# Optimization experiments

Hardware: AMD Instinct MI355X
Metric: run time of the kernel (lower is better)

The kernel has to match this reference:

```python
import jax, jax.numpy as jnp
import numpy as np
from jax import lax

EPS = 1e-5
N_CROPS = 501
CROP_W = 500
RF = 65          # temporal receptive field
KS = 15          # conv1 kernel size
POOL = 3


def _bn(x, g, b, m, v, axis=1):
    shp = [1] * x.ndim
    shp[axis] = -1
    inv = g.reshape(shp) / jnp.sqrt(v.reshape(shp) + EPS)
    return (x - m.reshape(shp)) * inv + b.reshape(shp)


def setup_inputs() -> dict:
    key = jax.random.key(0)
    ks = jax.random.split(key, 16)
    B, C_IN, CH, T = 16, 1, 22, 1001
    F = 36
    OUT = 4
    FLAT = F * 43  # 1548 (corrected fc in_features; repo constant 504 is inconsistent)
    d = {
        "x": jax.random.normal(ks[0], (B, C_IN, CH, T), jnp.float32),
        # temporal conv [1,65]
        "w_t": jax.random.normal(ks[1], (F, 1, 1, RF), jnp.float32) * 0.1,
        "b_t": jax.random.normal(ks[2], (F,), jnp.float32) * 0.1,
        "bn_t_g": jax.random.uniform(ks[3], (F,), jnp.float32, 0.5, 1.5),
        "bn_t_b": jax.random.normal(ks[4], (F,), jnp.float32) * 0.1,
        "bn_t_m": jax.random.normal(ks[5], (F,), jnp.float32) * 0.1,
        "bn_t_v": jax.random.uniform(ks[6], (F,), jnp.float32, 0.5, 1.5),
        # spatial conv [22,1]
        "w_s": jax.random.normal(ks[7], (F, F, CH, 1), jnp.float32) * 0.05,
        "b_s": jax.random.normal(ks[8], (F,), jnp.float32) * 0.1,
        "bn_s_g": jax.random.uniform(ks[9], (F,), jnp.float32, 0.5, 1.5),
        "bn_s_b": jax.random.normal(ks[10], (F,), jnp.float32) * 0.1,
        "bn_s_m": jax.random.normal(ks[11], (F,), jnp.float32) * 0.1,
        "bn_s_v": jax.random.uniform(ks[12], (F,), jnp.float32, 0.5, 1.5),
        # conv1 [1,15] (as 1-D conv over time)
        "w_c": jax.random.normal(ks[13], (F, F, KS), jnp.float32) * 0.05,
        "b_c": jax.random.normal(ks[14], (F,), jnp.float32) * 0.1,
        "bn_c_g": jnp.ones((F,), jnp.float32),
        "bn_c_b": jnp.zeros((F,), jnp.float32),
        "bn_c_m": jnp.zeros((F,), jnp.float32),
        "bn_c_v": jnp.ones((F,), jnp.float32),
        # fc
        "w_fc": jax.random.normal(ks[15], (OUT, FLAT), jnp.float32) * 0.02,
        "b_fc": jnp.zeros((OUT,), jnp.float32),
    }
    return d


def reference(x, w_t, b_t, bn_t_g, bn_t_b, bn_t_m, bn_t_v,
              w_s, b_s, bn_s_g, bn_s_b, bn_s_m, bn_s_v,
              w_c, b_c, bn_c_g, bn_c_b, bn_c_m, bn_c_v,
              w_fc, b_fc):
    B = x.shape[0]
    F = w_t.shape[0]
    OUT = b_fc.shape[0]

    # temporal + spatial conv/BN/ELU are shift-invariant -> compute once over full T
    h = lax.conv_general_dilated(x, w_t, (1, 1), 'VALID',
                                 dimension_numbers=('NCHW', 'OIHW', 'NCHW'))
    h = h + b_t[None, :, None, None]                       # [B,36,22,937]
    h = jax.nn.elu(_bn(h, bn_t_g, bn_t_b, bn_t_m, bn_t_v))
    h = lax.conv_general_dilated(h, w_s, (1, 1), 'VALID',
                                 dimension_numbers=('NCHW', 'OIHW', 'NCHW'))
    h = h + b_s[None, :, None, None]                       # [B,36,1,937]
    h = jax.nn.elu(_bn(h, bn_s_g, bn_s_b, bn_s_m, bn_s_v))
    h = h[:, :, 0, :]                                      # [B,36,937]

    TW = CROP_W - RF + 1  # 436: temporal width of each crop after temporal conv

    def crop_logits(i):
        sl = lax.dynamic_slice_in_dim(h, i, TW, axis=2)    # [B,36,436]
        p1 = sl[:, :, :435].reshape(B, F, 145, POOL).mean(-1)  # avgpool1 -> [B,36,145]
        c = lax.conv_general_dilated(p1, w_c, (1,), 'VALID',
                                     dimension_numbers=('NCH', 'OIH', 'NCH'))
        c = c + b_c[None, :, None]                          # [B,36,131]
        c = jax.nn.elu(_bn(c, bn_c_g, bn_c_b, bn_c_m, bn_c_v))
        p2 = c[:, :, :129].reshape(B, F, 43, POOL).mean(-1)  # avgpool2 -> [B,36,43]
        flat = p2.reshape(B, -1)                            # [B,1548]
        return flat @ w_fc.T + b_fc                         # [B,OUT]

    def step(acc, i):
        return acc + crop_logits(i), None

    init = jnp.zeros((B, OUT), x.dtype)
    total, _ = lax.scan(step, init, jnp.arange(N_CROPS))
    return total / N_CROPS
```

## Files before the change

### kernel.cpp

```cpp
#include <hip/hip_runtime.h>

#define EPS 1e-5f
#define B 16
#define CH 22
#define T_IN 1001
#define F 36
#define RF 65
#define T1 937
#define FC 792
#define KW 99
#define UN 885
#define PSTR 1072
#define PSPAN 304
#define KS 15
#define GN 295
#define WN 129
#define M43 43
#define BF 576

#define H2_OFF  0
#define P_OFF   539712
#define EP_OFF  1157184
#define S_OFF   5235264
#define WTT_OFF 5260032
#define WST_OFF 5262372
#define WCT_OFF 5290884
#define BN_OFF  5310324
#define H1_OFF  5310592

__device__ __forceinline__ float elu_f(float v) {
    return v > 0.f ? v : (__expf(v) - 1.f);
}

__global__ __launch_bounds__(256) void k_prep(
    const float* __restrict__ w_t, const float* __restrict__ w_s,
    const float* __restrict__ w_c,
    const float* __restrict__ b_t, const float* __restrict__ g_t,
    const float* __restrict__ be_t,const float* __restrict__ m_t,
    const float* __restrict__ v_t,
    const float* __restrict__ b_s, const float* __restrict__ g_s,
    const float* __restrict__ be_s,const float* __restrict__ m_s,
    const float* __restrict__ v_s,
    const float* __restrict__ b_c, const float* __restrict__ g_c,
    const float* __restrict__ be_c,const float* __restrict__ m_c,
    const float* __restrict__ v_c,
    float* __restrict__ wtT, float* __restrict__ wsT,
    float* __restrict__ wcT, float* __restrict__ bnz)
{
    int i = blockIdx.x * 256 + threadIdx.x;
    if (i < F * RF)     { int k = i / F,  fi = i % F; wtT[i] = w_t[fi * RF + k]; }
    if (i < FC * F)     { int fc = i / F, fo = i % F; wsT[i] = w_s[fo * FC + fc]; }
    if (i < F * KS * F) { int fk = i / F, fo = i % F; int f = fk / KS, k = fk % KS;
                          wcT[i] = w_c[(fo * F + f) * KS + k]; }
    if (i < F) {
        float s1 = g_t[i] * rsqrtf(v_t[i] + EPS);
        bnz[i]          = s1;
        bnz[F + i]      = (b_t[i] - m_t[i]) * s1 + be_t[i];
        float s2 = g_s[i] * rsqrtf(v_s[i] + EPS);
        bnz[2 * F + i]  = s2;
        bnz[3 * F + i]  = (b_s[i] - m_s[i]) * s2 + be_s[i];
        float s3 = g_c[i] * rsqrtf(v_c[i] + EPS);
        bnz[4 * F + i]  = s3;
        bnz[5 * F + i]  = (b_c[i] - m_c[i]) * s3 + be_c[i];
    }
}

__global__ __launch_bounds__(256) void k_tconv(
    const float* __restrict__ x, const float* __restrict__ wtT,
    const float* __restrict__ bnz, float* __restrict__ h1,
    int t_base, int TS, int TSeff)
{
    const int tloc = blockIdx.x * 256 + threadIdx.x;
    const int b = blockIdx.z, ch = blockIdx.y;
    int t = t_base + tloc;
    int tc = t < (T1 - 1) ? t : (T1 - 1);
    const float* xp = x + (b * CH + ch) * T_IN + tc;

    float acc[F];
    #pragma unroll
    for (int j = 0; j < F; ++j) acc[j] = 0.f;

    #pragma unroll 5
    for (int k = 0; k < RF; ++k) {
        float xv = xp[k];
        const float* wr = wtT + k * F;
        #pragma unroll
        for (int j = 0; j < F; ++j) acc[j] += xv * wr[j];
    }

    if (tloc < TSeff) {
        #pragma unroll
        for (int j = 0; j < F; ++j) {
            float s1 = bnz[j], o1 = bnz[F + j];
            h1[((size_t)(b * F + j) * CH + ch) * TS + tloc] =
                elu_f(acc[j] * s1 + o1);
        }
    }
}

__global__ __launch_bounds__(512) void k_sconv(
    const float* __restrict__ h1, const float* __restrict__ wsT,
    const float* __restrict__ bnz, float* __restrict__ h2,
    int t_base, int TS, int TSeff)
{
    __shared__ float Ls[8 * F * 64];
    const int tid = threadIdx.x;
    const int lane = tid & 63;
    const int w = __builtin_amdgcn_readfirstlane(tid >> 6);
    const int b = blockIdx.y;
    const int tl0 = blockIdx.x * 64;
    int tl = tl0 + lane;
    int tlc = tl < (TSeff - 1) ? tl : (TSeff - 1);

    const float* hq = h1 + ((size_t)b * FC + w * KW) * TS + tlc;
    const float* wb = wsT + (w * KW) * F;

    float acc[F];
    #pragma unroll
    for (int j = 0; j < F; ++j) acc[j] = 0.f;

    #pragma unroll 3
    for (int fc = 0; fc < KW; ++fc) {
        float hv = hq[(size_t)fc * TS];
        const float* wr = wb + fc * F;
        #pragma unroll
        for (int j = 0; j < F; ++j) acc[j] += hv * wr[j];
    }

    #pragma unroll
    for (int j = 0; j < F; ++j) Ls[(w * F + j) * 64 + lane] = acc[j];
    __syncthreads();

    for (int i = tid; i < F * 64; i += 512) {
        float s = 0.f;
        #pragma unroll
        for (int wq = 0; wq < 8; ++wq) s += Ls[wq * (F * 64) + i];
        int fo = i >> 6;
        int tloc2 = tl0 + (i & 63);
        int tg = t_base + tloc2;
        if (tloc2 < TSeff) {
            float s2 = bnz[2 * F + fo], o2 = bnz[3 * F + fo];
            h2[(b * F + fo) * T1 + tg] = elu_f(s * s2 + o2);
        }
    }
}

__global__ __launch_bounds__(256) void k_pool(
    const float* __restrict__ h2, float* __restrict__ P)
{
    const int bf = blockIdx.x;
    const float* hr = h2 + (size_t)bf * T1;
    for (int u = threadIdx.x; u < PSTR; u += 256) {
        float a = 0.f;
        #pragma unroll
        for (int d = 0; d < 3; ++d) {
            int s = u + d; if (s > T1 - 1) s = T1 - 1;
            a += hr[s];
        }
        P[(size_t)bf * PSTR + u] = a * (1.f / 3.f);
    }
}

__global__ __launch_bounds__(256) void k_qconv(
    const float* __restrict__ P, const float* __restrict__ wcT,
    float* __restrict__ Ep)
{
    __shared__ float Ps[5 * PSPAN];
    const int tid = threadIdx.x;
    const int slice = blockIdx.y, b = blockIdx.z;
    const int u0 = blockIdx.x * 256;
    const int f_base = slice < 4 ? slice * 5 : 20 + (slice - 4) * 4;
    const int nf     = slice < 4 ? 5 : 4;

    for (int i = tid; i < nf * PSPAN; i += 256) {
        int fl = i / PSPAN, j = i % PSPAN;
        Ps[i] = P[(size_t)(b * F + f_base + fl) * PSTR + u0 + j];
    }
    __syncthreads();

    const int lu = tid;

    float acc[F];
    #pragma unroll
    for (int j = 0; j < F; ++j) acc[j] = 0.f;

    for (int fl = 0; fl < nf; ++fl) {
        const int pb = fl * PSPAN + lu;
        #pragma unroll 5
        for (int k = 0; k < KS; ++k) {
            float pv = Ps[pb + 3 * k];
            const float* wr = wcT + ((f_base + fl) * KS + k) * F;
            #pragma unroll
            for (int j = 0; j < F; ++j) acc[j] += pv * wr[j];
        }
    }

    int u_g = u0 + lu;
    if (u_g < UN) {
        #pragma unroll
        for (int j = 0; j < F; ++j)
            Ep[(((size_t)slice * B + b) * F + j) * UN + u_g] = acc[j];
    }
}

__global__ __launch_bounds__(256) void k_wins(
    const float* __restrict__ Ep, const float* __restrict__ bnz,
    float* __restrict__ S)
{
    __shared__ float Es[UN];
    __shared__ float G[GN];
    __shared__ float Ws[WN];
    const int tid = threadIdx.x;
    const int bf = blockIdx.x;
    const int f = bf % F;
    const float sc = bnz[4 * F + f];
    const float oc = bnz[5 * F + f];
    for (int i = tid; i < UN; i += 256) {
        float s = 0.f;
        #pragma unroll
        for (int sl = 0; sl < 8; ++sl)
            s += Ep[((size_t)sl * BF + bf) * UN + i];
        Es[i] = elu_f(s * sc + oc);
    }
    __syncthreads();
    for (int q = tid; q < GN; q += 256)
        G[q] = Es[3 * q] + Es[3 * q + 1] + Es[3 * q + 2];
    __syncthreads();
    if (tid < WN) {
        float a = 0.f;
        for (int q = tid; q < tid + 167; ++q) a += G[q];
        Ws[tid] = a;
    }
    __syncthreads();
    if (tid < M43)
        S[bf * M43 + tid] = (Ws[3 * tid] + Ws[3 * tid + 1] + Ws[3 * tid + 2]) * (1.f / 3.f);
}

__global__ __launch_bounds__(256) void k_fc(
    const float* __restrict__ S, const float* __restrict__ w_fc,
    const float* __restrict__ b_fc, float* __restrict__ out)
{
    const int b = blockIdx.x;
    const int o = threadIdx.x >> 6;
    const int lane = threadIdx.x & 63;
    float acc = 0.f;
    for (int n = lane; n < F * M43; n += 64)
        acc += w_fc[o * (F * M43) + n] * S[b * (F * M43) + n];
    #pragma unroll
    for (int off = 32; off > 0; off >>= 1)
        acc += __shfl_down(acc, off, 64);
    if (lane == 0) out[b * 4 + o] = acc * (1.f / 501.f) + b_fc[o];
}

extern "C" void kernel_launch(void* const* d_in, const int* in_sizes, int n_in,
                              void* d_out, int out_size, void* d_ws, size_t ws_size,
                              hipStream_t stream) {
    const float* x    = (const float*)d_in[0];
    const float* w_t  = (const float*)d_in[1];
    const float* b_t  = (const float*)d_in[2];
    const float* g_t  = (const float*)d_in[3];
    const float* be_t = (const float*)d_in[4];
    const float* m_t  = (const float*)d_in[5];
    const float* v_t  = (const float*)d_in[6];
    const float* w_s  = (const float*)d_in[7];
    const float* b_s  = (const float*)d_in[8];
    const float* g_s  = (const float*)d_in[9];
    const float* be_s = (const float*)d_in[10];
    const float* m_s  = (const float*)d_in[11];
    const float* v_s  = (const float*)d_in[12];
    const float* w_c  = (const float*)d_in[13];
    const float* b_c  = (const float*)d_in[14];
    const float* g_c  = (const float*)d_in[15];
    const float* be_c = (const float*)d_in[16];
    const float* m_c  = (const float*)d_in[17];
    const float* v_c  = (const float*)d_in[18];
    const float* w_fc = (const float*)d_in[19];
    const float* b_fc = (const float*)d_in[20];

    float* ws  = (float*)d_ws;
    float* h2  = ws + H2_OFF;
    float* P   = ws + P_OFF;
    float* Ep  = ws + EP_OFF;
    float* S   = ws + S_OFF;
    float* wtT = ws + WTT_OFF;
    float* wsT = ws + WST_OFF;
    float* wcT = ws + WCT_OFF;
    float* bnz = ws + BN_OFF;
    float* h1  = ws + H1_OFF;
    float* out = (float*)d_out;

    long long availF = (long long)(ws_size / 4) - (long long)H1_OFF;
    long long tsl = availF / (B * FC);
    int TS;
    if (tsl >= T1) TS = T1;
    else { TS = (int)(tsl & ~63LL); if (TS < 64) TS = 64; }
    int nslab = (T1 + TS - 1) / TS;

    k_prep<<<dim3(112), 256, 0, stream>>>(
        w_t, w_s, w_c, b_t, g_t, be_t, m_t, v_t,
        b_s, g_s, be_s, m_s, v_s, b_c, g_c, be_c, m_c, v_c,
        wtT, wsT, wcT, bnz);

    for (int sl = 0; sl < nslab; ++sl) {
        int t_base = sl * TS;
        int TSeff = T1 - t_base; if (TSeff > TS) TSeff = TS;
        k_tconv<<<dim3((TSeff + 255) / 256, CH, B), 256, 0, stream>>>(
            x, wtT, bnz, h1, t_base, TS, TSeff);
        k_sconv<<<dim3((TSeff + 63) / 64, B), 512, 0, stream>>>(
            h1, wsT, bnz, h2, t_base, TS, TSeff);
    }

    k_pool<<<dim3(BF), 256, 0, stream>>>(h2, P);
    k_qconv<<<dim3(4, 8, B), 256, 0, stream>>>(P, wcT, Ep);
    k_wins<<<dim3(BF), 256, 0, stream>>>(Ep, bnz, S);
    k_fc<<<dim3(B), 256, 0, stream>>>(S, w_fc, b_fc, out);
}
```

Measured before the change: 185.2 us.

## Fuse pooling into qconv and FC into window kernel; raise unroll factors

Removes the standalone pooling kernel by computing the 3-tap average directly while staging h2 into shared memory in k_qconv. Removes the FC kernel by having each (b,f) block in k_wins dot its 43 pooled values with the matching FC weights and atomically add into the output, which k_prep initialises with the bias. Also raises loop unroll factors in the temporal and spatial conv kernels. This saves two launches and the P/S intermediate round trips, at the cost of float atomics (nondeterministic summation order) and possible register pressure from the larger unrolls.

```diff
diff --git a/kernel.cpp b/kernel.cpp
--- a/kernel.cpp
+++ b/kernel.cpp
@@ -10,23 +10,21 @@
 #define FC 792
 #define KW 99
 #define UN 885
-#define PSTR 1072
 #define PSPAN 304
 #define KS 15
 #define GN 295
 #define WN 129
 #define M43 43
 #define BF 576
+#define FLAT 1548
 
 #define H2_OFF  0
-#define P_OFF   539712
-#define EP_OFF  1157184
-#define S_OFF   5235264
-#define WTT_OFF 5260032
-#define WST_OFF 5262372
-#define WCT_OFF 5290884
-#define BN_OFF  5310324
-#define H1_OFF  5310592
+#define EP_OFF  539712
+#define WTT_OFF 4617792
+#define WST_OFF 4620132
+#define WCT_OFF 4648644
+#define BN_OFF  4668084
+#define H1_OFF  4668352
 
 __device__ __forceinline__ float elu_f(float v) {
     return v > 0.f ? v : (__expf(v) - 1.f);
@@ -43,9 +41,10 @@
     const float* __restrict__ v_s,
     const float* __restrict__ b_c, const float* __restrict__ g_c,
     const float* __restrict__ be_c,const float* __restrict__ m_c,
-    const float* __restrict__ v_c,
+    const float* __restrict__ v_c, const float* __restrict__ b_fc,
     float* __restrict__ wtT, float* __restrict__ wsT,
-    float* __restrict__ wcT, float* __restrict__ bnz)
+    float* __restrict__ wcT, float* __restrict__ bnz,
+    float* __restrict__ out)
 {
     int i = blockIdx.x * 256 + threadIdx.x;
     if (i < F * RF)     { int k = i / F,  fi = i % F; wtT[i] = w_t[fi * RF + k]; }
@@ -63,6 +62,7 @@
         bnz[4 * F + i]  = s3;
         bnz[5 * F + i]  = (b_c[i] - m_c[i]) * s3 + be_c[i];
     }
+    if (i < B * 4) out[i] = b_fc[i & 3];
 }
 
 __global__ __launch_bounds__(256) void k_tconv(
@@ -80,7 +80,7 @@
     #pragma unroll
     for (int j = 0; j < F; ++j) acc[j] = 0.f;
 
-    #pragma unroll 5
+    #pragma unroll 13
     for (int k = 0; k < RF; ++k) {
         float xv = xp[k];
         const float* wr = wtT + k * F;
@@ -119,7 +119,7 @@
     #pragma unroll
     for (int j = 0; j < F; ++j) acc[j] = 0.f;
 
-    #pragma unroll 3
+    #pragma unroll 9
     for (int fc = 0; fc < KW; ++fc) {
         float hv = hq[(size_t)fc * TS];
         const float* wr = wb + fc * F;
@@ -145,24 +145,8 @@
     }
 }
 
-__global__ __launch_bounds__(256) void k_pool(
-    const float* __restrict__ h2, float* __restrict__ P)
-{
-    const int bf = blockIdx.x;
-    const float* hr = h2 + (size_t)bf * T1;
-    for (int u = threadIdx.x; u < PSTR; u += 256) {
-        float a = 0.f;
-        #pragma unroll
-        for (int d = 0; d < 3; ++d) {
-            int s = u + d; if (s > T1 - 1) s = T1 - 1;
-            a += hr[s];
-        }
-        P[(size_t)bf * PSTR + u] = a * (1.f / 3.f);
-    }
-}
-
 __global__ __launch_bounds__(256) void k_qconv(
-    const float* __restrict__ P, const float* __restrict__ wcT,
+    const float* __restrict__ h2, const float* __restrict__ wcT,
     float* __restrict__ Ep)
 {
     __shared__ float Ps[5 * PSPAN];
@@ -174,7 +158,12 @@
 
     for (int i = tid; i < nf * PSPAN; i += 256) {
         int fl = i / PSPAN, j = i % PSPAN;
-        Ps[i] = P[(size_t)(b * F + f_base + fl) * PSTR + u0 + j];
+        const float* hr = h2 + (size_t)(b * F + f_base + fl) * T1;
+        int s = u0 + j;
+        int s0 = s     < T1 - 1 ? s     : T1 - 1;
+        int s1 = s + 1 < T1 - 1 ? s + 1 : T1 - 1;
+        int s2 = s + 2 < T1 - 1 ? s + 2 : T1 - 1;
+        Ps[i] = (hr[s0] + hr[s1] + hr[s2]) * (1.f / 3.f);
     }
     __syncthreads();
 
@@ -205,14 +194,15 @@
 
 __global__ __launch_bounds__(256) void k_wins(
     const float* __restrict__ Ep, const float* __restrict__ bnz,
-    float* __restrict__ S)
+    const float* __restrict__ w_fc, float* __restrict__ out)
 {
     __shared__ float Es[UN];
     __shared__ float G[GN];
     __shared__ float Ws[WN];
+    __shared__ float Sm[M43];
     const int tid = threadIdx.x;
     const int bf = blockIdx.x;
-    const int f = bf % F;
+    const int b = bf / F, f = bf % F;
     const float sc = bnz[4 * F + f];
     const float oc = bnz[5 * F + f];
     for (int i = tid; i < UN; i += 256) {
@@ -233,23 +223,15 @@
     }
     __syncthreads();
     if (tid < M43)
-        S[bf * M43 + tid] = (Ws[3 * tid] + Ws[3 * tid + 1] + Ws[3 * tid + 2]) * (1.f / 3.f);
-}
-
-__global__ __launch_bounds__(256) void k_fc(
-    const float* __restrict__ S, const float* __restrict__ w_fc,
-    const float* __restrict__ b_fc, float* __restrict__ out)
-{
-    const int b = blockIdx.x;
-    const int o = threadIdx.x >> 6;
-    const int lane = threadIdx.x & 63;
-    float acc = 0.f;
-    for (int n = lane; n < F * M43; n += 64)
-        acc += w_fc[o * (F * M43) + n] * S[b * (F * M43) + n];
-    #pragma unroll
-    for (int off = 32; off > 0; off >>= 1)
-        acc += __shfl_down(acc, off, 64);
-    if (lane == 0) out[b * 4 + o] = acc * (1.f / 501.f) + b_fc[o];
+        Sm[tid] = (Ws[3 * tid] + Ws[3 * tid + 1] + Ws[3 * tid + 2]) * (1.f / 3.f);
+    __syncthreads();
+    if (tid < 4) {
+        const float* wr = w_fc + tid * FLAT + f * M43;
+        float a = 0.f;
+        #pragma unroll 43
+        for (int m = 0; m < M43; ++m) a += Sm[m] * wr[m];
+        atomicAdd(&out[b * 4 + tid], a * (1.f / 501.f));
+    }
 }
 
 extern "C" void kernel_launch(void* const* d_in, const int* in_sizes, int n_in,
@@ -279,9 +261,7 @@
 
     float* ws  = (float*)d_ws;
     float* h2  = ws + H2_OFF;
-    float* P   = ws + P_OFF;
     float* Ep  = ws + EP_OFF;
-    float* S   = ws + S_OFF;
     float* wtT = ws + WTT_OFF;
     float* wsT = ws + WST_OFF;
     float* wcT = ws + WCT_OFF;
@@ -298,8 +278,8 @@
 
     k_prep<<<dim3(112), 256, 0, stream>>>(
         w_t, w_s, w_c, b_t, g_t, be_t, m_t, v_t,
-        b_s, g_s, be_s, m_s, v_s, b_c, g_c, be_c, m_c, v_c,
-        wtT, wsT, wcT, bnz);
+        b_s, g_s, be_s, m_s, v_s, b_c, g_c, be_c, m_c, v_c, b_fc,
+        wtT, wsT, wcT, bnz, out);
 
     for (int sl = 0; sl < nslab; ++sl) {
         int t_base = sl * TS;
@@ -310,8 +290,6 @@
             h1, wsT, bnz, h2, t_base, TS, TSeff);
     }
 
-    k_pool<<<dim3(BF), 256, 0, stream>>>(h2, P);
-    k_qconv<<<dim3(4, 8, B), 256, 0, stream>>>(P, wcT, Ep);
-    k_wins<<<dim3(BF), 256, 0, stream>>>(Ep, bnz, S);
-    k_fc<<<dim3(B), 256, 0, stream>>>(S, w_fc, b_fc, out);
-}
+    k_qconv<<<dim3(4, 8, B), 256, 0, stream>>>(h2, wcT, Ep);
+    k_wins<<<dim3(BF), 256, 0, stream>>>(Ep, bnz, w_fc, out);
+}
```

Result: faster. 179.5 us (-3.1%).
